# Kernel optimization log

Measured on AMD Instinct MI355X. Metric: run time of the kernel, lower is better.

The kernel has to match this reference:

```python
import jax, jax.numpy as jnp
import numpy as np

N = 10000      # nodes
E = 160000     # edges
G = 128        # graphs in batch
DIMS = [16, 32, 32]  # in_channels, then conv output dims
HID = 25       # edge-MLP hidden width
EPS = 1e-5     # batch-norm eps


def setup_inputs() -> dict:
    key = jax.random.key(0)
    ks = iter(jax.random.split(key, 40))
    inp = {}
    inp["x"] = jax.random.normal(next(ks), (N, DIMS[0]), dtype=jnp.float32)
    inp["edge_attr"] = jax.random.uniform(next(ks), (E, 3), dtype=jnp.float32)
    inp["edge_index"] = jax.random.randint(next(ks), (2, E), 0, N, dtype=jnp.int32)
    inp["batch"] = jnp.sort(jax.random.randint(next(ks), (N,), 0, G, dtype=jnp.int32))
    for i in range(2):
        din, dout = DIMS[i], DIMS[i + 1]
        inp[f"w1_{i}"] = jax.random.normal(next(ks), (3, HID), dtype=jnp.float32) * 0.3
        inp[f"b1_{i}"] = jnp.zeros((HID,), jnp.float32)
        inp[f"g_{i}"] = jnp.ones((HID,), jnp.float32)
        inp[f"be_{i}"] = jnp.zeros((HID,), jnp.float32)
        inp[f"w2_{i}"] = jax.random.normal(next(ks), (HID, din * dout), dtype=jnp.float32) * 0.05
        inp[f"b2_{i}"] = jnp.zeros((din * dout,), jnp.float32)
        inp[f"wr_{i}"] = jax.random.normal(next(ks), (din, dout), dtype=jnp.float32) * 0.1
        inp[f"bc_{i}"] = jnp.zeros((dout,), jnp.float32)
    inp["wfc"] = jax.random.normal(next(ks), (DIMS[-1], 1), dtype=jnp.float32) * 0.1
    inp["bfc"] = jnp.zeros((1,), jnp.float32)
    return inp


def _ecn(x, edge_attr, layers, wfc, bfc, edge_index, batch):
    src, dst = edge_index[0], edge_index[1]
    deg = jax.ops.segment_sum(jnp.ones((E,), x.dtype), dst, num_segments=N)
    deg = jnp.clip(deg, 1.0)[:, None]          # [N,1], PyG mean clamps count>=1
    for (w1, b1, g, be, w2, b2, wr, bc) in layers:
        # edge MLP: Linear(3,25) -> BatchNorm(batch stats) -> ReLU -> Linear(25, in*out)
        h = edge_attr @ w1 + b1                 # [E,25]
        mu = h.mean(axis=0)
        var = h.var(axis=0)
        h = (h - mu) * jax.lax.rsqrt(var + EPS) * g + be
        h = jax.nn.relu(h)
        w = (h @ w2 + b2).reshape(E, x.shape[1], -1)   # [E,in,out] per-edge weights
        msg = jnp.einsum('ei,eio->eo', x[src], w)      # gather + per-edge matmul
        agg = jax.ops.segment_sum(msg, dst, num_segments=N) / deg  # scatter-mean
        x = agg + x @ wr + bc                   # root transform + bias
        x = jax.nn.elu(x)
    # global mean pool over graphs
    gsum = jax.ops.segment_sum(x, batch, num_segments=G)
    gcnt = jnp.clip(jax.ops.segment_sum(jnp.ones((N,), x.dtype), batch, num_segments=G), 1.0)
    pooled = gsum / gcnt[:, None]               # [G, dims[-1]]
    return pooled @ wfc + bfc                   # fc MLP last layer is plain Linear


def reference(x, edge_attr, edge_index, batch,
              w1_0, b1_0, g_0, be_0, w2_0, b2_0, wr_0, bc_0,
              w1_1, b1_1, g_1, be_1, w2_1, b2_1, wr_1, bc_1,
              wfc, bfc):
    layers = [
        (w1_0, b1_0, g_0, be_0, w2_0, b2_0, wr_0, bc_0),
        (w1_1, b1_1, g_1, be_1, w2_1, b2_1, wr_1, bc_1),
    ]
    return _ecn(x, edge_attr, layers, wfc, bfc, edge_index, batch)
```

## Files before the change

kernel.cpp:

```cpp
#include <hip/hip_runtime.h>
#include <math.h>

#define NN   10000
#define EE   160000
#define GG   128
#define HIDK 25
#define KROWS 32
#define KB   28
#define DOUT 32
#define EPSBN 1e-5f
#define PREPB 1024
#define WPACKN (KROWS * 16 * DOUT + KROWS * 32 * DOUT)
#define MAXD 48

#define OFF_CUR   0
#define OFF_GSUM  10016
#define OFF_GCNT  14112
#define ZERO_FLOATS 14240
#define OFF_MOP   14240
#define OFF_W1F0  26528
#define OFF_B1F0  26608
#define OFF_W1F1  26640
#define OFF_B1F1  26720
#define OFF_EA    26752
#define OFF_WB0   1946752
#define OFF_WB1   1963136
#define OFF_X1    1995904
#define TOTAL_FLOATS 2315904


__device__ inline float wave_red(float v) {
    for (int off = 32; off; off >>= 1) v += __shfl_down(v, off);
    return v;
}

template <int DIN>
__device__ inline void wpack(int idx, const float* __restrict__ w2,
                             const float* __restrict__ b2,
                             const float* __restrict__ wr,
                             const float* __restrict__ bc,
                             float* __restrict__ wbig) {
    int k = idx / (DIN * DOUT);
    int rem = idx - k * (DIN * DOUT);
    int i4 = rem / (4 * DOUT);
    int rem2 = rem - i4 * (4 * DOUT);
    int o = rem2 >> 2, c = rem2 & 3;
    int i = i4 * 4 + c;
    float v = 0.f;
    if (k < HIDK) v = w2[(k * DIN + i) * DOUT + o];
    else if (k == HIDK) v = b2[i * DOUT + o];
    else if (k == HIDK + 1) v = wr[i * DOUT + o];
    else if (k == HIDK + 2) v = (i == 0) ? bc[o] : 0.f;
    wbig[idx] = v;
}

__global__ void k_prep(const float* __restrict__ ea, const int* __restrict__ ei,
                       const int* __restrict__ batch,
                       const float* __restrict__ w2_0, const float* __restrict__ b2_0,
                       const float* __restrict__ wr_0, const float* __restrict__ bc_0,
                       const float* __restrict__ w2_1, const float* __restrict__ b2_1,
                       const float* __restrict__ wr_1, const float* __restrict__ bc_1,
                       float* __restrict__ mop, int* __restrict__ cur,
                       int* __restrict__ gcnt, float* __restrict__ eab,
                       float* __restrict__ wb0, float* __restrict__ wb1) {
    __shared__ float ls[4][9];
    int t = threadIdx.x;
    int idx = blockIdx.x * 256 + t;

    if (idx < KROWS * 16 * DOUT) wpack<16>(idx, w2_0, b2_0, wr_0, bc_0, wb0);
    else if (idx < WPACKN) wpack<32>(idx - KROWS * 16 * DOUT, w2_1, b2_1, wr_1, bc_1, wb1);

    float s[9];
#pragma unroll
    for (int j = 0; j < 9; j++) s[j] = 0.f;
    if (idx < EE) {
        float a0 = ea[3 * idx], a1 = ea[3 * idx + 1], a2 = ea[3 * idx + 2];
        s[0] = a0; s[1] = a1; s[2] = a2;
        s[3] = a0 * a0; s[4] = a0 * a1; s[5] = a0 * a2;
        s[6] = a1 * a1; s[7] = a1 * a2; s[8] = a2 * a2;
        int d = ei[EE + idx];
        int pos = atomicAdd(cur + d, 1);
        if (pos < MAXD) {
            int slot = d * MAXD + pos;
            float4 av = { a0, a1, a2, __int_as_float(ei[idx]) };
            *(float4*)(eab + 4 * (size_t)slot) = av;
        }
    }
    if (idx < NN) atomicAdd(gcnt + batch[idx], 1);

    int w = t >> 6, lane = t & 63;
#pragma unroll
    for (int j = 0; j < 9; j++) {
        float r = wave_red(s[j]);
        if (lane == 0) ls[w][j] = r;
    }
    __syncthreads();
    if (t < 9) mop[blockIdx.x * 12 + t] = ls[0][t] + ls[1][t] + ls[2][t] + ls[3][t];
}

__global__ void k_fold(const float* __restrict__ mop,
                       const float* __restrict__ w1_0, const float* __restrict__ b1_0,
                       const float* __restrict__ g_0, const float* __restrict__ be_0,
                       const float* __restrict__ w1_1, const float* __restrict__ b1_1,
                       const float* __restrict__ g_1, const float* __restrict__ be_1,
                       float* __restrict__ w1f0, float* __restrict__ b1f0,
                       float* __restrict__ w1f1, float* __restrict__ b1f1) {
    __shared__ float ls[4][9];
    __shared__ float mo[9];
    int t = threadIdx.x;
    float s[9];
#pragma unroll
    for (int j = 0; j < 9; j++) s[j] = 0.f;
    for (int b = t; b < PREPB; b += 256) {
#pragma unroll
        for (int j = 0; j < 9; j++) s[j] += mop[b * 12 + j];
    }
    int w = t >> 6, lane = t & 63;
#pragma unroll
    for (int j = 0; j < 9; j++) {
        float r = wave_red(s[j]);
        if (lane == 0) ls[w][j] = r;
    }
    __syncthreads();
    if (t < 9) mo[t] = ls[0][t] + ls[1][t] + ls[2][t] + ls[3][t];
    __syncthreads();
    if (t < 64) {
        int grp = t >> 5, j = t & 31;
        if (j < HIDK) {
            const float* w1 = grp ? w1_1 : w1_0;
            const float* b1 = grp ? b1_1 : b1_0;
            const float* g  = grp ? g_1  : g_0;
            const float* be = grp ? be_1 : be_0;
            float* w1f = grp ? w1f1 : w1f0;
            float* b1f = grp ? b1f1 : b1f0;
            const float inv = 1.0f / (float)EE;
            float m0 = mo[0] * inv, m1 = mo[1] * inv, m2 = mo[2] * inv;
            float c00 = mo[3] * inv - m0 * m0, c01 = mo[4] * inv - m0 * m1;
            float c02 = mo[5] * inv - m0 * m2, c11 = mo[6] * inv - m1 * m1;
            float c12 = mo[7] * inv - m1 * m2, c22 = mo[8] * inv - m2 * m2;
            float w0 = w1[j], wa = w1[25 + j], wb = w1[50 + j];
            float mean = m0 * w0 + m1 * wa + m2 * wb + b1[j];
            float var = w0 * w0 * c00 + wa * wa * c11 + wb * wb * c22
                      + 2.f * (w0 * wa * c01 + w0 * wb * c02 + wa * wb * c12);
            float sc = g[j] * rsqrtf(var + EPSBN);
            w1f[j] = w0 * sc; w1f[25 + j] = wa * sc; w1f[50 + j] = wb * sc;
            b1f[j] = (b1[j] - mean) * sc + be[j];
        }
    }
}

template <int DIN, int KPL, bool FINAL>
__global__ __launch_bounds__(256, 6)
void k_fused(const int* __restrict__ cnt,
             const float* __restrict__ eab,
             const float* __restrict__ w1f, const float* __restrict__ b1f,
             const float* __restrict__ wbig, const float* __restrict__ xin,
             const int* __restrict__ batch,
             float* __restrict__ xout, float* __restrict__ gsum) {
    __shared__ __align__(16) float Slds[4][KROWS][DIN];
    __shared__ float Olds[4][4][DOUT];
    __shared__ __align__(16) float hb[4][2][2][32];
    int t = threadIdx.x;
    int w = t >> 6, lane = t & 63;
    int n = blockIdx.x * 4 + w;
    int dg = cnt[n];
    int start = n * MAXD;
    int end = start + (dg > MAXD ? MAXD : dg);

    int il = lane & (DIN - 1);
    int kh = lane / DIN;
    int kme = lane & 31;
    int half = lane >> 5;

    float c0 = 0.f, c1 = 0.f, c2 = 0.f, c3 = 0.f;
    if (kme < HIDK) {
        c0 = w1f[kme]; c1 = w1f[25 + kme]; c2 = w1f[50 + kme]; c3 = b1f[kme];
    } else if (kme == HIDK) {
        c3 = 1.0f;
    }

    float x_own = xin[n * DIN + il];

    float s[KPL];
#pragma unroll
    for (int j = 0; j < KPL; j++) s[j] = 0.f;

    const float4* ea4 = (const float4*)eab;

    int p = start;
    int vB0 = 0, vB1 = 0;
    float xA = 0.f, xB = 0.f;
    float4 av1 = {0.f, 0.f, 0.f, 0.f};
    int buf = 0;

    if (p < end) {
        vB0 = (p + 1 < end); int qB0 = vB0 ? p + 1 : p;
        float4 av0 = ea4[half ? qB0 : p];
        int p1 = p + 2;
        if (p1 < end) {
            vB1 = (p1 + 1 < end); int qB1 = vB1 ? p1 + 1 : p1;
            av1 = ea4[half ? qB1 : p1];
        }
        int me0 = __float_as_int(av0.w);
        int sA0 = __shfl(me0, 0), sB0 = __shfl(me0, 32);
        xA = xin[sA0 * DIN + il];
        xB = xin[sB0 * DIN + il];
        float hv = av0.x * c0 + av0.y * c1 + av0.z * c2 + c3;
        hv = hv > 0.f ? hv : 0.f;
        hb[w][0][half][kme] = hv;
    }
    while (p < end) {
        int p1 = p + 2, p2 = p + 4;
        float4 av2 = {0.f, 0.f, 0.f, 0.f};
        int vB2 = 0;
        if (p2 < end) {
            vB2 = (p2 + 1 < end); int qB2 = vB2 ? p2 + 1 : p2;
            av2 = ea4[half ? qB2 : p2];
        }
        int me1 = __float_as_int(av1.w);
        int sA1 = __shfl(me1, 0), sB1 = __shfl(me1, 32);
        float xAn = 0.f, xBn = 0.f;
        if (p1 < end) { xAn = xin[sA1 * DIN + il]; xBn = xin[sB1 * DIN + il]; }
        const float4* hA4 = (const float4*)&hb[w][buf][0][kh * KPL];
        const float4* hB4 = (const float4*)&hb[w][buf][1][kh * KPL];
        float4 ha[KPL / 4], hc[KPL / 4];
#pragma unroll
        for (int j4 = 0; j4 < KPL / 4; j4++) { ha[j4] = hA4[j4]; hc[j4] = hB4[j4]; }
        if (p1 < end) {
            float hv = av1.x * c0 + av1.y * c1 + av1.z * c2 + c3;
            hv = hv > 0.f ? hv : 0.f;
            hb[w][buf ^ 1][half][kme] = hv;
        }
        float xBm = vB0 ? xB : 0.f;
#pragma unroll
        for (int j4 = 0; j4 < KPL / 4; j4++) {
            s[j4 * 4 + 0] += ha[j4].x * xA; s[j4 * 4 + 1] += ha[j4].y * xA;
            s[j4 * 4 + 2] += ha[j4].z * xA; s[j4 * 4 + 3] += ha[j4].w * xA;
        }
#pragma unroll
        for (int j4 = 0; j4 < KPL / 4; j4++) {
            s[j4 * 4 + 0] += hc[j4].x * xBm; s[j4 * 4 + 1] += hc[j4].y * xBm;
            s[j4 * 4 + 2] += hc[j4].z * xBm; s[j4 * 4 + 3] += hc[j4].w * xBm;
        }
        p = p1;
        vB0 = vB1; vB1 = vB2;
        xA = xAn; xB = xBn; av1 = av2;
        buf ^= 1;
    }
#pragma unroll
    for (int j = 0; j < KPL; j++)
        Slds[w][kh * KPL + j][il] = s[j];
    float dmul = (float)dg; if (dmul < 1.f) dmul = 1.f;
    if (half == 0) {
        Slds[w][26][il] = dmul * x_own;
        Slds[w][27][il] = (il == 0) ? dmul : 0.f;
    }
    __syncthreads();

    {
        int o = lane & 31, hf = lane >> 5;
        constexpr int I4H = DIN / 8;
        const float4* wb4 = (const float4*)wbig;
        float a0 = 0.f, a1 = 0.f, a2 = 0.f, a3 = 0.f;
        int kbase = w * (KB / 4);
#pragma unroll
        for (int kk = 0; kk < KB / 4; kk++) {
            int k = kbase + kk;
#pragma unroll
            for (int j = 0; j < I4H; j++) {
                int i4 = hf * I4H + j;
                float4 wv = wb4[(k * (DIN / 4) + i4) * 32 + o];
                float4 s0 = *(const float4*)&Slds[0][k][i4 * 4];
                float4 s1 = *(const float4*)&Slds[1][k][i4 * 4];
                float4 s2 = *(const float4*)&Slds[2][k][i4 * 4];
                float4 s3 = *(const float4*)&Slds[3][k][i4 * 4];
                a0 += s0.x * wv.x + s0.y * wv.y + s0.z * wv.z + s0.w * wv.w;
                a1 += s1.x * wv.x + s1.y * wv.y + s1.z * wv.z + s1.w * wv.w;
                a2 += s2.x * wv.x + s2.y * wv.y + s2.z * wv.z + s2.w * wv.w;
                a3 += s3.x * wv.x + s3.y * wv.y + s3.z * wv.z + s3.w * wv.w;
            }
        }
        a0 += __shfl_xor(a0, 32);
        a1 += __shfl_xor(a1, 32);
        a2 += __shfl_xor(a2, 32);
        a3 += __shfl_xor(a3, 32);
        if (hf == 0) {
            Olds[w][0][o] = a0; Olds[w][1][o] = a1;
            Olds[w][2][o] = a2; Olds[w][3][o] = a3;
        }
    }
    __syncthreads();

    if (t < 4 * DOUT) {
        int m = t >> 5, o2 = t & 31;
        int n2 = blockIdx.x * 4 + m;
        float d = (float)cnt[n2]; if (d < 1.f) d = 1.f;
        float r = (Olds[0][m][o2] + Olds[1][m][o2] + Olds[2][m][o2] + Olds[3][m][o2]) / d;
        r = r > 0.f ? r : expm1f(r);
        if (FINAL) atomicAdd(gsum + batch[n2] * DOUT + o2, r);
        else xout[n2 * DOUT + o2] = r;
    }
}

__global__ void k_fc(const float* __restrict__ gsum, const int* __restrict__ gcnt,
                     const float* __restrict__ wfc, const float* __restrict__ bfc,
                     float* __restrict__ out) {
    int g = threadIdx.x;
    if (g >= GG) return;
    float c = (float)gcnt[g]; if (c < 1.f) c = 1.f;
    float acc = 0.f;
#pragma unroll
    for (int o = 0; o < DOUT; o++) acc += gsum[g * DOUT + o] * wfc[o];
    out[g] = acc / c + bfc[0];
}

extern "C" void kernel_launch(void* const* d_in, const int* in_sizes, int n_in,
                              void* d_out, int out_size, void* d_ws, size_t ws_size,
                              hipStream_t stream) {
    const float* x     = (const float*)d_in[0];
    const float* ea    = (const float*)d_in[1];
    const int*   ei    = (const int*)d_in[2];
    const int*   batch = (const int*)d_in[3];
    const float* w1_0 = (const float*)d_in[4];
    const float* b1_0 = (const float*)d_in[5];
    const float* g_0  = (const float*)d_in[6];
    const float* be_0 = (const float*)d_in[7];
    const float* w2_0 = (const float*)d_in[8];
    const float* b2_0 = (const float*)d_in[9];
    const float* wr_0 = (const float*)d_in[10];
    const float* bc_0 = (const float*)d_in[11];
    const float* w1_1 = (const float*)d_in[12];
    const float* b1_1 = (const float*)d_in[13];
    const float* g_1  = (const float*)d_in[14];
    const float* be_1 = (const float*)d_in[15];
    const float* w2_1 = (const float*)d_in[16];
    const float* b2_1 = (const float*)d_in[17];
    const float* wr_1 = (const float*)d_in[18];
    const float* bc_1 = (const float*)d_in[19];
    const float* wfc  = (const float*)d_in[20];
    const float* bfc  = (const float*)d_in[21];

    float* ws    = (float*)d_ws;
    int*   cur   = (int*)(ws + OFF_CUR);
    float* gsum  = ws + OFF_GSUM;
    int*   gcnt  = (int*)(ws + OFF_GCNT);
    float* mop   = ws + OFF_MOP;
    float* w1f0  = ws + OFF_W1F0;
    float* b1f0  = ws + OFF_B1F0;
    float* w1f1  = ws + OFF_W1F1;
    float* b1f1  = ws + OFF_B1F1;
    float* eab   = ws + OFF_EA;
    float* wb0   = ws + OFF_WB0;
    float* wb1   = ws + OFF_WB1;
    float* x1    = ws + OFF_X1;

    hipMemsetAsync(ws, 0, (size_t)ZERO_FLOATS * sizeof(float), stream);

    k_prep<<<PREPB, 256, 0, stream>>>(ea, ei, batch,
                                      w2_0, b2_0, wr_0, bc_0, w2_1, b2_1, wr_1, bc_1,
                                      mop, cur, gcnt, eab, wb0, wb1);
    k_fold<<<1, 256, 0, stream>>>(mop, w1_0, b1_0, g_0, be_0, w1_1, b1_1, g_1, be_1,
                                  w1f0, b1f0, w1f1, b1f1);

    k_fused<16, 8, false><<<NN / 4, 256, 0, stream>>>(cur, eab, w1f0, b1f0,
                                                      wb0, x, batch, x1, gsum);
    k_fused<32, 16, true><<<NN / 4, 256, 0, stream>>>(cur, eab, w1f1, b1f1,
                                                      wb1, x1, batch, nullptr, gsum);

    k_fc<<<1, 128, 0, stream>>>(gsum, gcnt, wfc, bfc, (float*)d_out);
}
```

Before: 194.9 us.

## Sort nodes by in-degree so each block processes similar-degree nodes

Builds a degree histogram in k_fold and a counting-sort permutation in a new k_perm kernel, then has both fused layer kernels pick their nodes through this permutation. The four waves in a block then see similar edge counts, which is meant to cut intra-block imbalance at the block-wide syncs. In exchange it adds one more launch, a serial prefix scan, global atomics, and scattered accesses to node rows. Nodes with degree above MAXD are clamped into the last bin.

```diff
diff --git a/kernel.cpp b/kernel.cpp
--- a/kernel.cpp
+++ b/kernel.cpp
@@ -16,17 +16,20 @@
 #define OFF_CUR   0
 #define OFF_GSUM  10016
 #define OFF_GCNT  14112
-#define ZERO_FLOATS 14240
-#define OFF_MOP   14240
-#define OFF_W1F0  26528
-#define OFF_B1F0  26608
-#define OFF_W1F1  26640
-#define OFF_B1F1  26720
-#define OFF_EA    26752
-#define OFF_WB0   1946752
-#define OFF_WB1   1963136
-#define OFF_X1    1995904
-#define TOTAL_FLOATS 2315904
+#define OFF_BINC  14240
+#define ZERO_FLOATS 14304
+#define OFF_MOP   14304
+#define OFF_W1F0  26592
+#define OFF_B1F0  26672
+#define OFF_W1F1  26704
+#define OFF_B1F1  26784
+#define OFF_BOFF  26816
+#define OFF_PERM  26880
+#define OFF_EA    36896
+#define OFF_WB0   1956896
+#define OFF_WB1   1973280
+#define OFF_X1    2006048
+#define TOTAL_FLOATS 2326048
 
 
 __device__ inline float wave_red(float v) {
@@ -99,15 +102,19 @@
 }
 
 __global__ void k_fold(const float* __restrict__ mop,
+                       const int* __restrict__ cur,
                        const float* __restrict__ w1_0, const float* __restrict__ b1_0,
                        const float* __restrict__ g_0, const float* __restrict__ be_0,
                        const float* __restrict__ w1_1, const float* __restrict__ b1_1,
                        const float* __restrict__ g_1, const float* __restrict__ be_1,
                        float* __restrict__ w1f0, float* __restrict__ b1f0,
-                       float* __restrict__ w1f1, float* __restrict__ b1f1) {
+                       float* __restrict__ w1f1, float* __restrict__ b1f1,
+                       int* __restrict__ binoff) {
     __shared__ float ls[4][9];
     __shared__ float mo[9];
+    __shared__ int hist[MAXD + 1];
     int t = threadIdx.x;
+    if (t <= MAXD) hist[t] = 0;
     float s[9];
 #pragma unroll
     for (int j = 0; j < 9; j++) s[j] = 0.f;
@@ -123,7 +130,15 @@
     }
     __syncthreads();
     if (t < 9) mo[t] = ls[0][t] + ls[1][t] + ls[2][t] + ls[3][t];
+    for (int nn = t; nn < NN; nn += 256) {
+        int d = cur[nn]; if (d > MAXD) d = MAXD;
+        atomicAdd(&hist[d], 1);
+    }
     __syncthreads();
+    if (t == 0) {
+        int run = 0;
+        for (int d = 0; d <= MAXD; d++) { binoff[d] = run; run += hist[d]; }
+    }
     if (t < 64) {
         int grp = t >> 5, j = t & 31;
         if (j < HIDK) {
@@ -149,9 +164,19 @@
     }
 }
 
+__global__ void k_perm(const int* __restrict__ cur, const int* __restrict__ binoff,
+                       int* __restrict__ binc, int* __restrict__ perm) {
+    int nn = blockIdx.x * 256 + threadIdx.x;
+    if (nn >= NN) return;
+    int d = cur[nn]; if (d > MAXD) d = MAXD;
+    int pos = atomicAdd(binc + d, 1);
+    perm[binoff[d] + pos] = nn;
+}
+
 template <int DIN, int KPL, bool FINAL>
 __global__ __launch_bounds__(256, 6)
 void k_fused(const int* __restrict__ cnt,
+             const int* __restrict__ perm,
              const float* __restrict__ eab,
              const float* __restrict__ w1f, const float* __restrict__ b1f,
              const float* __restrict__ wbig, const float* __restrict__ xin,
@@ -162,7 +187,7 @@
     __shared__ __align__(16) float hb[4][2][2][32];
     int t = threadIdx.x;
     int w = t >> 6, lane = t & 63;
-    int n = blockIdx.x * 4 + w;
+    int n = perm[blockIdx.x * 4 + w];
     int dg = cnt[n];
     int start = n * MAXD;
     int end = start + (dg > MAXD ? MAXD : dg);
@@ -293,7 +318,7 @@
 
     if (t < 4 * DOUT) {
         int m = t >> 5, o2 = t & 31;
-        int n2 = blockIdx.x * 4 + m;
+        int n2 = perm[blockIdx.x * 4 + m];
         float d = (float)cnt[n2]; if (d < 1.f) d = 1.f;
         float r = (Olds[0][m][o2] + Olds[1][m][o2] + Olds[2][m][o2] + Olds[3][m][o2]) / d;
         r = r > 0.f ? r : expm1f(r);
@@ -344,11 +369,14 @@
     int*   cur   = (int*)(ws + OFF_CUR);
     float* gsum  = ws + OFF_GSUM;
     int*   gcnt  = (int*)(ws + OFF_GCNT);
+    int*   binc  = (int*)(ws + OFF_BINC);
     float* mop   = ws + OFF_MOP;
     float* w1f0  = ws + OFF_W1F0;
     float* b1f0  = ws + OFF_B1F0;
     float* w1f1  = ws + OFF_W1F1;
     float* b1f1  = ws + OFF_B1F1;
+    int*   boff  = (int*)(ws + OFF_BOFF);
+    int*   perm  = (int*)(ws + OFF_PERM);
     float* eab   = ws + OFF_EA;
     float* wb0   = ws + OFF_WB0;
     float* wb1   = ws + OFF_WB1;
@@ -359,12 +387,14 @@
     k_prep<<<PREPB, 256, 0, stream>>>(ea, ei, batch,
                                       w2_0, b2_0, wr_0, bc_0, w2_1, b2_1, wr_1, bc_1,
                                       mop, cur, gcnt, eab, wb0, wb1);
-    k_fold<<<1, 256, 0, stream>>>(mop, w1_0, b1_0, g_0, be_0, w1_1, b1_1, g_1, be_1,
-                                  w1f0, b1f0, w1f1, b1f1);
-
-    k_fused<16, 8, false><<<NN / 4, 256, 0, stream>>>(cur, eab, w1f0, b1f0,
+    k_fold<<<1, 256, 0, stream>>>(mop, cur,
+                                  w1_0, b1_0, g_0, be_0, w1_1, b1_1, g_1, be_1,
+                                  w1f0, b1f0, w1f1, b1f1, boff);
+    k_perm<<<(NN + 255) / 256, 256, 0, stream>>>(cur, boff, binc, perm);
+
+    k_fused<16, 8, false><<<NN / 4, 256, 0, stream>>>(cur, perm, eab, w1f0, b1f0,
                                                       wb0, x, batch, x1, gsum);
-    k_fused<32, 16, true><<<NN / 4, 256, 0, stream>>>(cur, eab, w1f1, b1f1,
+    k_fused<32, 16, true><<<NN / 4, 256, 0, stream>>>(cur, perm, eab, w1f1, b1f1,
                                                       wb1, x1, batch, nullptr, gsum);
 
     k_fc<<<1, 128, 0, stream>>>(gsum, gcnt, wfc, bfc, (float*)d_out);
```

New measurement: 227.7 us. 16.8% more time.
